# Kernel tuning notes

Measured on AMD Instinct MI355X. Metric: run time of the kernel, lower is better.

## Reference

```python
import jax, jax.numpy as jnp
import numpy as np

ALPHA = 0.2  # LeakyReLU negative slope
NEG_PAD = jnp.float32(-2**31)
N, IN_F, OUT_F = 8192, 512, 64


def setup_inputs() -> dict:
    key = jax.random.key(0)
    k1, k2, k3, k4 = jax.random.split(key, 4)
    h = jax.random.normal(k1, (N, IN_F), dtype=jnp.float32)
    adj = jax.random.randint(k2, (N, N), 0, 2, dtype=jnp.int32)
    # xavier_uniform with gain=1.414
    gain = 1.414
    limW = gain * np.sqrt(6.0 / (IN_F + OUT_F))
    W = jax.random.uniform(k3, (IN_F, OUT_F), dtype=jnp.float32, minval=-limW, maxval=limW)
    lima = gain * np.sqrt(6.0 / (2 * OUT_F + 1))
    a = jax.random.uniform(k4, (2 * OUT_F, 1), dtype=jnp.float32, minval=-lima, maxval=lima)
    return {"h": h, "adj": adj, "W": W, "a": a}


def reference(h, adj, W, a):
    Wh = h @ W                                   # [N, F']
    Wh1 = Wh @ a[:OUT_F, :]                      # [N, 1]
    Wh2 = Wh @ a[OUT_F:, :]                      # [N, 1]
    e = jax.nn.leaky_relu(Wh1 + Wh2.T, negative_slope=ALPHA)  # [N, N]
    attention = jnp.where(adj > 0, e, NEG_PAD)
    attention = jax.nn.softmax(attention, axis=1)
    # dropout in eval mode -> identity
    h_prime = attention @ Wh                     # [N, F']
    return jax.nn.elu(h_prime)                   # concat=True branch
```

## Files before the change

### kernel.cpp

```cpp
#include <hip/hip_runtime.h>
#include <cstdint>
#include <cstddef>

#define LRALPHA 0.2f

typedef _Float16 half8 __attribute__((ext_vector_type(8)));
typedef float f32x4 __attribute__((ext_vector_type(4)));

__global__ __launch_bounds__(256) void k0_bitpack(const int* __restrict__ adj,
                                                  unsigned char* __restrict__ bits8)
{
  const int nb = 8192 * 1024;
  const int stride = gridDim.x * 256;
  for (int b = blockIdx.x * 256 + threadIdx.x; b < nb; b += stride) {
    const int4* p = reinterpret_cast<const int4*>(adj + (size_t)b * 8);
    const int4 x = p[0], y = p[1];
    unsigned m = (x.x > 0 ? 1u : 0u) | (x.y > 0 ? 2u : 0u)
               | (x.z > 0 ? 4u : 0u) | (x.w > 0 ? 8u : 0u)
               | (y.x > 0 ? 16u : 0u) | (y.y > 0 ? 32u : 0u)
               | (y.z > 0 ? 64u : 0u) | (y.w > 0 ? 128u : 0u);
    bits8[b] = (unsigned char)m;
  }
}

__global__ __launch_bounds__(256) void k1_wh(
    const float* __restrict__ h, const float* __restrict__ W, const float* __restrict__ a,
    _Float16* __restrict__ whTsw, float* __restrict__ wh1, float* __restrict__ wh2)
{
  __shared__ __align__(16) float h_lds[32][34];
  __shared__ __align__(16) float w_lds[32][64];
  __shared__ __align__(16) _Float16 whT_l[64][32];

  const int t = threadIdx.x;
  const int tx = t & 15, ty = t >> 4;
  const int i0 = blockIdx.x * 32;

  const int hrow = t >> 3, hk4 = (t & 7) * 4;
  const int wk = t >> 3, wc = (t & 7) * 8;

  float acc00 = 0, acc01 = 0, acc02 = 0, acc03 = 0;
  float acc10 = 0, acc11 = 0, acc12 = 0, acc13 = 0;

  float4 hv  = *reinterpret_cast<const float4*>(&h[(size_t)(i0 + hrow) * 512 + hk4]);
  float4 wv0 = *reinterpret_cast<const float4*>(&W[(size_t)wk * 64 + wc]);
  float4 wv1 = *reinterpret_cast<const float4*>(&W[(size_t)wk * 64 + wc + 4]);

  for (int k0 = 0; k0 < 512; k0 += 32) {
    h_lds[hk4 + 0][hrow] = hv.x;
    h_lds[hk4 + 1][hrow] = hv.y;
    h_lds[hk4 + 2][hrow] = hv.z;
    h_lds[hk4 + 3][hrow] = hv.w;
    *reinterpret_cast<float4*>(&w_lds[wk][wc])     = wv0;
    *reinterpret_cast<float4*>(&w_lds[wk][wc + 4]) = wv1;
    __syncthreads();
    if (k0 + 32 < 512) {
      hv  = *reinterpret_cast<const float4*>(&h[(size_t)(i0 + hrow) * 512 + k0 + 32 + hk4]);
      wv0 = *reinterpret_cast<const float4*>(&W[(size_t)(k0 + 32 + wk) * 64 + wc]);
      wv1 = *reinterpret_cast<const float4*>(&W[(size_t)(k0 + 32 + wk) * 64 + wc + 4]);
    }
#pragma unroll
    for (int kk = 0; kk < 32; ++kk) {
      float2 av = *reinterpret_cast<const float2*>(&h_lds[kk][ty * 2]);
      float4 bv = *reinterpret_cast<const float4*>(&w_lds[kk][tx * 4]);
      acc00 += av.x * bv.x; acc01 += av.x * bv.y; acc02 += av.x * bv.z; acc03 += av.x * bv.w;
      acc10 += av.y * bv.x; acc11 += av.y * bv.y; acc12 += av.y * bv.z; acc13 += av.y * bv.w;
    }
    __syncthreads();
  }

  const float a10 = a[tx * 4 + 0], a11 = a[tx * 4 + 1], a12 = a[tx * 4 + 2], a13 = a[tx * 4 + 3];
  const float a20 = a[64 + tx * 4 + 0], a21 = a[64 + tx * 4 + 1], a22 = a[64 + tx * 4 + 2], a23 = a[64 + tx * 4 + 3];
  float s1_0 = acc00 * a10 + acc01 * a11 + acc02 * a12 + acc03 * a13;
  float s1_1 = acc10 * a10 + acc11 * a11 + acc12 * a12 + acc13 * a13;
  float s2_0 = acc00 * a20 + acc01 * a21 + acc02 * a22 + acc03 * a23;
  float s2_1 = acc10 * a20 + acc11 * a21 + acc12 * a22 + acc13 * a23;
#pragma unroll
  for (int m = 1; m < 16; m <<= 1) {
    s1_0 += __shfl_xor(s1_0, m); s1_1 += __shfl_xor(s1_1, m);
    s2_0 += __shfl_xor(s2_0, m); s2_1 += __shfl_xor(s2_1, m);
  }
  if (tx == 0) {
    wh1[i0 + ty * 2 + 0] = s1_0; wh1[i0 + ty * 2 + 1] = s1_1;
    wh2[i0 + ty * 2 + 0] = s2_0; wh2[i0 + ty * 2 + 1] = s2_1;
  }

  whT_l[tx * 4 + 0][ty * 2 + 0] = (_Float16)acc00;
  whT_l[tx * 4 + 1][ty * 2 + 0] = (_Float16)acc01;
  whT_l[tx * 4 + 2][ty * 2 + 0] = (_Float16)acc02;
  whT_l[tx * 4 + 3][ty * 2 + 0] = (_Float16)acc03;
  whT_l[tx * 4 + 0][ty * 2 + 1] = (_Float16)acc10;
  whT_l[tx * 4 + 1][ty * 2 + 1] = (_Float16)acc11;
  whT_l[tx * 4 + 2][ty * 2 + 1] = (_Float16)acc12;
  whT_l[tx * 4 + 3][ty * 2 + 1] = (_Float16)acc13;
  __syncthreads();
  {
    const int cp = t >> 6, cc = (t >> 2) & 15, ks = t & 3;
    half8 v = *reinterpret_cast<const half8*>(&whT_l[cp * 16 + cc][ks * 8]);
    *reinterpret_cast<half8*>(&whTsw[(size_t)(i0 >> 5) * 2048 + cp * 512 + (cc * 4 + ks) * 8]) = v;
  }
}

__global__ __launch_bounds__(256) void k1b_max(const float* __restrict__ wh2,
                                               float* __restrict__ G)
{
  const int t = threadIdx.x;
  float m = -1e30f;
  for (int i = t; i < 8192; i += 256) m = fmaxf(m, wh2[i]);
#pragma unroll
  for (int mask = 32; mask >= 1; mask >>= 1) m = fmaxf(m, __shfl_xor(m, mask));
  __shared__ float wm[4];
  if ((t & 63) == 0) wm[t >> 6] = m;
  __syncthreads();
  if (t == 0) G[0] = fmaxf(fmaxf(wm[0], wm[1]), fmaxf(wm[2], wm[3]));
}

__global__ __launch_bounds__(512) void k2_attn(
    const unsigned char* __restrict__ bits8, const _Float16* __restrict__ whTsw,
    const float* __restrict__ wh1, const float* __restrict__ wh2,
    const float* __restrict__ Gp, float* __restrict__ out)
{
  __shared__ __align__(16) float Osm[8][16][64];
  __shared__ float Dsm[8][16];

  const int t = threadIdx.x;
  const int lane = t & 63;
  const int w = t >> 6;
  const int c = lane & 15;
  const int ks = lane >> 4;
  const int i0 = blockIdx.x * 16;

  const float Gv = Gp[0];
  const float w1r = wh1[i0 + c];
  const float mx = w1r + Gv;
  const float mh = fmaxf(mx, LRALPHA * mx);

  const unsigned char* mp = bits8 + (size_t)(i0 + c) * 1024 + w * 128 + ks;
  const float* wh2p = wh2 + w * 1024 + ks * 8;
  const _Float16* bp = whTsw + (size_t)(w * 32) * 2048 + (c * 4 + ks) * 8;

  f32x4 acc0 = {0.f,0.f,0.f,0.f}, acc1 = {0.f,0.f,0.f,0.f};
  f32x4 acc2 = {0.f,0.f,0.f,0.f}, acc3 = {0.f,0.f,0.f,0.f};
  float ps = 0.f;

  unsigned Am, Bm;
  float4 Aw0, Aw1, Bw0, Bw1;
  half8 Ab0, Ab1, Ab2, Ab3, Bb0, Bb1, Bb2, Bb3;

#define LOADSET(P, CI) do {                                                     \
    P##m  = mp[(CI) * 4];                                                       \
    P##w0 = *reinterpret_cast<const float4*>(wh2p + (CI) * 32);                 \
    P##w1 = *reinterpret_cast<const float4*>(wh2p + (CI) * 32 + 4);             \
    P##b0 = *reinterpret_cast<const half8*>(bp + (size_t)(CI) * 2048);          \
    P##b1 = *reinterpret_cast<const half8*>(bp + (size_t)(CI) * 2048 + 512);    \
    P##b2 = *reinterpret_cast<const half8*>(bp + (size_t)(CI) * 2048 + 1024);   \
    P##b3 = *reinterpret_cast<const half8*>(bp + (size_t)(CI) * 2048 + 1536); } while (0)

#define BODY(P, NEXTCI) do {                                                    \
    const unsigned cm = P##m;                                                   \
    const float4 cw0 = P##w0, cw1 = P##w1;                                      \
    const half8 cb0 = P##b0, cb1 = P##b1, cb2 = P##b2, cb3 = P##b3;             \
    if ((NEXTCI) < 32) LOADSET(P, NEXTCI);                                      \
    half8 af;                                                                   \
    { float s_ = w1r + cw0.x; s_ = fmaxf(s_, LRALPHA*s_);                       \
      float p_ = (cm & 1u)   ? __expf(s_ - mh) : 0.f; ps += p_; af[0] = (_Float16)p_; } \
    { float s_ = w1r + cw0.y; s_ = fmaxf(s_, LRALPHA*s_);                       \
      float p_ = (cm & 2u)   ? __expf(s_ - mh) : 0.f; ps += p_; af[1] = (_Float16)p_; } \
    { float s_ = w1r + cw0.z; s_ = fmaxf(s_, LRALPHA*s_);                       \
      float p_ = (cm & 4u)   ? __expf(s_ - mh) : 0.f; ps += p_; af[2] = (_Float16)p_; } \
    { float s_ = w1r + cw0.w; s_ = fmaxf(s_, LRALPHA*s_);                       \
      float p_ = (cm & 8u)   ? __expf(s_ - mh) : 0.f; ps += p_; af[3] = (_Float16)p_; } \
    { float s_ = w1r + cw1.x; s_ = fmaxf(s_, LRALPHA*s_);                       \
      float p_ = (cm & 16u)  ? __expf(s_ - mh) : 0.f; ps += p_; af[4] = (_Float16)p_; } \
    { float s_ = w1r + cw1.y; s_ = fmaxf(s_, LRALPHA*s_);                       \
      float p_ = (cm & 32u)  ? __expf(s_ - mh) : 0.f; ps += p_; af[5] = (_Float16)p_; } \
    { float s_ = w1r + cw1.z; s_ = fmaxf(s_, LRALPHA*s_);                       \
      float p_ = (cm & 64u)  ? __expf(s_ - mh) : 0.f; ps += p_; af[6] = (_Float16)p_; } \
    { float s_ = w1r + cw1.w; s_ = fmaxf(s_, LRALPHA*s_);                       \
      float p_ = (cm & 128u) ? __expf(s_ - mh) : 0.f; ps += p_; af[7] = (_Float16)p_; } \
    acc0 = __builtin_amdgcn_mfma_f32_16x16x32_f16(af, cb0, acc0, 0, 0, 0);      \
    acc1 = __builtin_amdgcn_mfma_f32_16x16x32_f16(af, cb1, acc1, 0, 0, 0);      \
    acc2 = __builtin_amdgcn_mfma_f32_16x16x32_f16(af, cb2, acc2, 0, 0, 0);      \
    acc3 = __builtin_amdgcn_mfma_f32_16x16x32_f16(af, cb3, acc3, 0, 0, 0);      \
  } while (0)

  LOADSET(A, 0);
  LOADSET(B, 1);

  for (int ci = 0; ci < 32; ci += 2) {
    BODY(A, ci + 2);
    BODY(B, ci + 3);
  }
#undef BODY
#undef LOADSET

  float r = ps;
  r += __shfl_xor(r, 16);
  r += __shfl_xor(r, 32);
  if (ks == 0) Dsm[w][c] = r;

#pragma unroll
  for (int q = 0; q < 4; ++q) {
    Osm[w][ks * 4 + q][ 0 + c] = acc0[q];
    Osm[w][ks * 4 + q][16 + c] = acc1[q];
    Osm[w][ks * 4 + q][32 + c] = acc2[q];
    Osm[w][ks * 4 + q][48 + c] = acc3[q];
  }
  __syncthreads();

  {
    const int row = t >> 5, c2 = (t & 31) * 2;
    float d = 0.f, sx = 0.f, sy = 0.f;
#pragma unroll
    for (int ww = 0; ww < 8; ++ww) {
      d  += Dsm[ww][row];
      float2 v = *reinterpret_cast<const float2*>(&Osm[ww][row][c2]);
      sx += v.x; sy += v.y;
    }
    const float inv = 1.0f / d;
    float ox = sx * inv, oy = sy * inv;
    ox = ox > 0.f ? ox : __expf(ox) - 1.f;
    oy = oy > 0.f ? oy : __expf(oy) - 1.f;
    float2 o = {ox, oy};
    *reinterpret_cast<float2*>(&out[(size_t)(i0 + row) * 64 + c2]) = o;
  }
}

extern "C" void kernel_launch(void* const* d_in, const int* in_sizes, int n_in,
                              void* d_out, int out_size, void* d_ws, size_t ws_size,
                              hipStream_t stream) {
  const float* h   = (const float*)d_in[0];
  const int*   adj = (const int*)d_in[1];
  const float* W   = (const float*)d_in[2];
  const float* a   = (const float*)d_in[3];
  float* out = (float*)d_out;

  char* ws = (char*)d_ws;
  _Float16* whTsw = (_Float16*)ws;
  float* wh1 = (float*)(ws + 0x100000);
  float* wh2 = (float*)(ws + 0x108000);
  float* G   = (float*)(ws + 0x110000);
  unsigned char* bits8 = (unsigned char*)(ws + 0x120000);

  k0_bitpack<<<dim3(2048), dim3(256), 0, stream>>>(adj, bits8);
  k1_wh<<<dim3(256), dim3(256), 0, stream>>>(h, W, a, whTsw, wh1, wh2);
  k1b_max<<<dim3(1), dim3(256), 0, stream>>>(wh2, G);
  k2_attn<<<dim3(512), dim3(512), 0, stream>>>(bits8, whTsw, wh1, wh2, G, out);
}
```

Measured before the change: 123.3 us.

## Split attention into score kernel writing fp16 P and separate PV MFMA kernel

Drops the adjacency bitpack pre-pass and the fused score+MFMA kernel. A new score kernel reads the int32 adjacency directly, computes the masked exponentials, and writes a full fp16 probability matrix plus per-stripe row-sum partials. A second kernel multiplies that matrix by Wh with MFMA, handling two row tiles per block. This decouples the exp-heavy scoring work from the MFMA work, but it adds a large intermediate write and re-read of the N×N fp16 matrix, far more than the packed bitmask it replaces.

```diff
diff --git a/kernel.cpp b/kernel.cpp
--- a/kernel.cpp
+++ b/kernel.cpp
@@ -6,22 +6,6 @@
 
 typedef _Float16 half8 __attribute__((ext_vector_type(8)));
 typedef float f32x4 __attribute__((ext_vector_type(4)));
-
-__global__ __launch_bounds__(256) void k0_bitpack(const int* __restrict__ adj,
-                                                  unsigned char* __restrict__ bits8)
-{
-  const int nb = 8192 * 1024;
-  const int stride = gridDim.x * 256;
-  for (int b = blockIdx.x * 256 + threadIdx.x; b < nb; b += stride) {
-    const int4* p = reinterpret_cast<const int4*>(adj + (size_t)b * 8);
-    const int4 x = p[0], y = p[1];
-    unsigned m = (x.x > 0 ? 1u : 0u) | (x.y > 0 ? 2u : 0u)
-               | (x.z > 0 ? 4u : 0u) | (x.w > 0 ? 8u : 0u)
-               | (y.x > 0 ? 16u : 0u) | (y.y > 0 ? 32u : 0u)
-               | (y.z > 0 ? 64u : 0u) | (y.w > 0 ? 128u : 0u);
-    bits8[b] = (unsigned char)m;
-  }
-}
 
 __global__ __launch_bounds__(256) void k1_wh(
     const float* __restrict__ h, const float* __restrict__ W, const float* __restrict__ a,
@@ -114,78 +98,122 @@
   if (t == 0) G[0] = fmaxf(fmaxf(wm[0], wm[1]), fmaxf(wm[2], wm[3]));
 }
 
-__global__ __launch_bounds__(512) void k2_attn(
-    const unsigned char* __restrict__ bits8, const _Float16* __restrict__ whTsw,
-    const float* __restrict__ wh1, const float* __restrict__ wh2,
-    const float* __restrict__ Gp, float* __restrict__ out)
-{
-  __shared__ __align__(16) float Osm[8][16][64];
-  __shared__ float Dsm[8][16];
-
+__global__ __launch_bounds__(256) void k2s_score(
+    const int* __restrict__ adj, const float* __restrict__ wh1,
+    const float* __restrict__ wh2, const float* __restrict__ Gp,
+    _Float16* __restrict__ P, float* __restrict__ Dpart)
+{
   const int t = threadIdx.x;
   const int lane = t & 63;
   const int w = t >> 6;
-  const int c = lane & 15;
-  const int ks = lane >> 4;
-  const int i0 = blockIdx.x * 16;
+  const int g = blockIdx.x * 4 + w;
+  const int tile = g >> 3;
+  const int stripe = g & 7;
+  const int c = lane & 15, ks = lane >> 4;
+  const int row = tile * 16 + c;
 
   const float Gv = Gp[0];
-  const float w1r = wh1[i0 + c];
+  const float w1r = wh1[row];
   const float mx = w1r + Gv;
   const float mh = fmaxf(mx, LRALPHA * mx);
 
-  const unsigned char* mp = bits8 + (size_t)(i0 + c) * 1024 + w * 128 + ks;
-  const float* wh2p = wh2 + w * 1024 + ks * 8;
-  const _Float16* bp = whTsw + (size_t)(w * 32) * 2048 + (c * 4 + ks) * 8;
-
-  f32x4 acc0 = {0.f,0.f,0.f,0.f}, acc1 = {0.f,0.f,0.f,0.f};
-  f32x4 acc2 = {0.f,0.f,0.f,0.f}, acc3 = {0.f,0.f,0.f,0.f};
+  const int*   ap = adj + (size_t)row * 8192 + stripe * 1024 + ks * 8;
+  const float* wp = wh2 + stripe * 1024 + ks * 8;
+  _Float16* pp = P + (size_t)(tile * 256 + stripe * 32) * 512 + (c * 4 + ks) * 8;
+
   float ps = 0.f;
 
-  unsigned Am, Bm;
+  int4 Aa0, Aa1, Ba0, Ba1;
   float4 Aw0, Aw1, Bw0, Bw1;
-  half8 Ab0, Ab1, Ab2, Ab3, Bb0, Bb1, Bb2, Bb3;
-
-#define LOADSET(P, CI) do {                                                     \
-    P##m  = mp[(CI) * 4];                                                       \
-    P##w0 = *reinterpret_cast<const float4*>(wh2p + (CI) * 32);                 \
-    P##w1 = *reinterpret_cast<const float4*>(wh2p + (CI) * 32 + 4);             \
-    P##b0 = *reinterpret_cast<const half8*>(bp + (size_t)(CI) * 2048);          \
-    P##b1 = *reinterpret_cast<const half8*>(bp + (size_t)(CI) * 2048 + 512);    \
-    P##b2 = *reinterpret_cast<const half8*>(bp + (size_t)(CI) * 2048 + 1024);   \
-    P##b3 = *reinterpret_cast<const half8*>(bp + (size_t)(CI) * 2048 + 1536); } while (0)
-
-#define BODY(P, NEXTCI) do {                                                    \
-    const unsigned cm = P##m;                                                   \
-    const float4 cw0 = P##w0, cw1 = P##w1;                                      \
-    const half8 cb0 = P##b0, cb1 = P##b1, cb2 = P##b2, cb3 = P##b3;             \
-    if ((NEXTCI) < 32) LOADSET(P, NEXTCI);                                      \
-    half8 af;                                                                   \
-    { float s_ = w1r + cw0.x; s_ = fmaxf(s_, LRALPHA*s_);                       \
-      float p_ = (cm & 1u)   ? __expf(s_ - mh) : 0.f; ps += p_; af[0] = (_Float16)p_; } \
-    { float s_ = w1r + cw0.y; s_ = fmaxf(s_, LRALPHA*s_);                       \
-      float p_ = (cm & 2u)   ? __expf(s_ - mh) : 0.f; ps += p_; af[1] = (_Float16)p_; } \
-    { float s_ = w1r + cw0.z; s_ = fmaxf(s_, LRALPHA*s_);                       \
-      float p_ = (cm & 4u)   ? __expf(s_ - mh) : 0.f; ps += p_; af[2] = (_Float16)p_; } \
-    { float s_ = w1r + cw0.w; s_ = fmaxf(s_, LRALPHA*s_);                       \
-      float p_ = (cm & 8u)   ? __expf(s_ - mh) : 0.f; ps += p_; af[3] = (_Float16)p_; } \
-    { float s_ = w1r + cw1.x; s_ = fmaxf(s_, LRALPHA*s_);                       \
-      float p_ = (cm & 16u)  ? __expf(s_ - mh) : 0.f; ps += p_; af[4] = (_Float16)p_; } \
-    { float s_ = w1r + cw1.y; s_ = fmaxf(s_, LRALPHA*s_);                       \
-      float p_ = (cm & 32u)  ? __expf(s_ - mh) : 0.f; ps += p_; af[5] = (_Float16)p_; } \
-    { float s_ = w1r + cw1.z; s_ = fmaxf(s_, LRALPHA*s_);                       \
-      float p_ = (cm & 64u)  ? __expf(s_ - mh) : 0.f; ps += p_; af[6] = (_Float16)p_; } \
-    { float s_ = w1r + cw1.w; s_ = fmaxf(s_, LRALPHA*s_);                       \
-      float p_ = (cm & 128u) ? __expf(s_ - mh) : 0.f; ps += p_; af[7] = (_Float16)p_; } \
-    acc0 = __builtin_amdgcn_mfma_f32_16x16x32_f16(af, cb0, acc0, 0, 0, 0);      \
-    acc1 = __builtin_amdgcn_mfma_f32_16x16x32_f16(af, cb1, acc1, 0, 0, 0);      \
-    acc2 = __builtin_amdgcn_mfma_f32_16x16x32_f16(af, cb2, acc2, 0, 0, 0);      \
-    acc3 = __builtin_amdgcn_mfma_f32_16x16x32_f16(af, cb3, acc3, 0, 0, 0);      \
-  } while (0)
+
+#define LOADSET(Q, CI) do {                                                     \
+    Q##a0 = *reinterpret_cast<const int4*>(ap + (CI) * 32);                     \
+    Q##a1 = *reinterpret_cast<const int4*>(ap + (CI) * 32 + 4);                 \
+    Q##w0 = *reinterpret_cast<const float4*>(wp + (CI) * 32);                   \
+    Q##w1 = *reinterpret_cast<const float4*>(wp + (CI) * 32 + 4); } while (0)
+
+#define SCORE(AV, WV, E) {                                                      \
+    float s_ = w1r + (WV);                                                      \
+    s_ = fmaxf(s_, LRALPHA * s_);                                               \
+    float p_ = ((AV) > 0) ? __expf(s_ - mh) : 0.f;                              \
+    ps += p_; pv[E] = (_Float16)p_; }
+
+#define BODY(Q, CI, NEXTCI) do {                                                \
+    const int4 a0 = Q##a0, a1 = Q##a1;                                          \
+    const float4 q0 = Q##w0, q1 = Q##w1;                                        \
+    if ((NEXTCI) < 32) LOADSET(Q, NEXTCI);                                      \
+    half8 pv;                                                                   \
+    SCORE(a0.x, q0.x, 0) SCORE(a0.y, q0.y, 1)                                   \
+    SCORE(a0.z, q0.z, 2) SCORE(a0.w, q0.w, 3)                                   \
+    SCORE(a1.x, q1.x, 4) SCORE(a1.y, q1.y, 5)                                   \
+    SCORE(a1.z, q1.z, 6) SCORE(a1.w, q1.w, 7)                                   \
+    *reinterpret_cast<half8*>(pp + (size_t)(CI) * 512) = pv; } while (0)
 
   LOADSET(A, 0);
   LOADSET(B, 1);
-
+  for (int ci = 0; ci < 32; ci += 2) {
+    BODY(A, ci, ci + 2);
+    BODY(B, ci + 1, ci + 3);
+  }
+#undef BODY
+#undef SCORE
+#undef LOADSET
+
+  float r = ps;
+  r += __shfl_xor(r, 16);
+  r += __shfl_xor(r, 32);
+  if (ks == 0) Dpart[(size_t)stripe * 8192 + row] = r;
+}
+
+__global__ __launch_bounds__(512) void k3_pv(
+    const _Float16* __restrict__ P, const _Float16* __restrict__ whTsw,
+    const float* __restrict__ Dpart, float* __restrict__ out)
+{
+  __shared__ __align__(16) float Osm[8][32][64];
+
+  const int t = threadIdx.x;
+  const int lane = t & 63;
+  const int w = t >> 6;
+  const int c = lane & 15, ks = lane >> 4;
+  const int tile0 = blockIdx.x * 2;
+  const int row0 = tile0 * 16;
+
+  const _Float16* pp0 = P + (size_t)(tile0 * 256 + w * 32) * 512 + (c * 4 + ks) * 8;
+  const _Float16* pp1 = pp0 + 256 * 512;
+  const _Float16* bp  = whTsw + (size_t)(w * 32) * 2048 + (c * 4 + ks) * 8;
+
+  f32x4 a00 = {0.f,0.f,0.f,0.f}, a01 = {0.f,0.f,0.f,0.f};
+  f32x4 a02 = {0.f,0.f,0.f,0.f}, a03 = {0.f,0.f,0.f,0.f};
+  f32x4 a10 = {0.f,0.f,0.f,0.f}, a11 = {0.f,0.f,0.f,0.f};
+  f32x4 a12 = {0.f,0.f,0.f,0.f}, a13 = {0.f,0.f,0.f,0.f};
+
+  half8 Aa, Az, Ab0, Ab1, Ab2, Ab3;
+  half8 Ba, Bz, Bb0, Bb1, Bb2, Bb3;
+
+#define LOADSET(Q, CI) do {                                                     \
+    Q##a  = *reinterpret_cast<const half8*>(pp0 + (size_t)(CI) * 512);          \
+    Q##z  = *reinterpret_cast<const half8*>(pp1 + (size_t)(CI) * 512);          \
+    Q##b0 = *reinterpret_cast<const half8*>(bp + (size_t)(CI) * 2048);          \
+    Q##b1 = *reinterpret_cast<const half8*>(bp + (size_t)(CI) * 2048 + 512);    \
+    Q##b2 = *reinterpret_cast<const half8*>(bp + (size_t)(CI) * 2048 + 1024);   \
+    Q##b3 = *reinterpret_cast<const half8*>(bp + (size_t)(CI) * 2048 + 1536); } while (0)
+
+#define BODY(Q, NEXTCI) do {                                                    \
+    const half8 fa = Q##a, fz = Q##z;                                           \
+    const half8 cb0 = Q##b0, cb1 = Q##b1, cb2 = Q##b2, cb3 = Q##b3;             \
+    if ((NEXTCI) < 32) LOADSET(Q, NEXTCI);                                      \
+    a00 = __builtin_amdgcn_mfma_f32_16x16x32_f16(fa, cb0, a00, 0, 0, 0);        \
+    a01 = __builtin_amdgcn_mfma_f32_16x16x32_f16(fa, cb1, a01, 0, 0, 0);        \
+    a02 = __builtin_amdgcn_mfma_f32_16x16x32_f16(fa, cb2, a02, 0, 0, 0);        \
+    a03 = __builtin_amdgcn_mfma_f32_16x16x32_f16(fa, cb3, a03, 0, 0, 0);        \
+    a10 = __builtin_amdgcn_mfma_f32_16x16x32_f16(fz, cb0, a10, 0, 0, 0);        \
+    a11 = __builtin_amdgcn_mfma_f32_16x16x32_f16(fz, cb1, a11, 0, 0, 0);        \
+    a12 = __builtin_amdgcn_mfma_f32_16x16x32_f16(fz, cb2, a12, 0, 0, 0);        \
+    a13 = __builtin_amdgcn_mfma_f32_16x16x32_f16(fz, cb3, a13, 0, 0, 0);        \
+  } while (0)
+
+  LOADSET(A, 0);
+  LOADSET(B, 1);
   for (int ci = 0; ci < 32; ci += 2) {
     BODY(A, ci + 2);
     BODY(B, ci + 3);
@@ -193,35 +221,38 @@
 #undef BODY
 #undef LOADSET
 
-  float r = ps;
-  r += __shfl_xor(r, 16);
-  r += __shfl_xor(r, 32);
-  if (ks == 0) Dsm[w][c] = r;
-
 #pragma unroll
   for (int q = 0; q < 4; ++q) {
-    Osm[w][ks * 4 + q][ 0 + c] = acc0[q];
-    Osm[w][ks * 4 + q][16 + c] = acc1[q];
-    Osm[w][ks * 4 + q][32 + c] = acc2[q];
-    Osm[w][ks * 4 + q][48 + c] = acc3[q];
+    Osm[w][ks * 4 + q][ 0 + c] = a00[q];
+    Osm[w][ks * 4 + q][16 + c] = a01[q];
+    Osm[w][ks * 4 + q][32 + c] = a02[q];
+    Osm[w][ks * 4 + q][48 + c] = a03[q];
+    Osm[w][16 + ks * 4 + q][ 0 + c] = a10[q];
+    Osm[w][16 + ks * 4 + q][16 + c] = a11[q];
+    Osm[w][16 + ks * 4 + q][32 + c] = a12[q];
+    Osm[w][16 + ks * 4 + q][48 + c] = a13[q];
   }
   __syncthreads();
 
   {
-    const int row = t >> 5, c2 = (t & 31) * 2;
-    float d = 0.f, sx = 0.f, sy = 0.f;
+    const int row = t >> 4, c4 = (t & 15) * 4;
+    float d = 0.f;
+#pragma unroll
+    for (int s = 0; s < 8; ++s) d += Dpart[(size_t)s * 8192 + row0 + row];
+    const float inv = 1.0f / d;
+    float sx = 0.f, sy = 0.f, sz = 0.f, sw = 0.f;
 #pragma unroll
     for (int ww = 0; ww < 8; ++ww) {
-      d  += Dsm[ww][row];
-      float2 v = *reinterpret_cast<const float2*>(&Osm[ww][row][c2]);
-      sx += v.x; sy += v.y;
+      float4 v = *reinterpret_cast<const float4*>(&Osm[ww][row][c4]);
+      sx += v.x; sy += v.y; sz += v.z; sw += v.w;
     }
-    const float inv = 1.0f / d;
-    float ox = sx * inv, oy = sy * inv;
-    ox = ox > 0.f ? ox : __expf(ox) - 1.f;
-    oy = oy > 0.f ? oy : __expf(oy) - 1.f;
-    float2 o = {ox, oy};
-    *reinterpret_cast<float2*>(&out[(size_t)(i0 + row) * 64 + c2]) = o;
+    float4 o;
+    o.x = sx * inv; o.y = sy * inv; o.z = sz * inv; o.w = sw * inv;
+    o.x = o.x > 0.f ? o.x : __expf(o.x) - 1.f;
+    o.y = o.y > 0.f ? o.y : __expf(o.y) - 1.f;
+    o.z = o.z > 0.f ? o.z : __expf(o.z) - 1.f;
+    o.w = o.w > 0.f ? o.w : __expf(o.w) - 1.f;
+    *reinterpret_cast<float4*>(&out[(size_t)(row0 + row) * 64 + c4]) = o;
   }
 }
 
@@ -236,13 +267,14 @@
 
   char* ws = (char*)d_ws;
   _Float16* whTsw = (_Float16*)ws;
-  float* wh1 = (float*)(ws + 0x100000);
-  float* wh2 = (float*)(ws + 0x108000);
-  float* G   = (float*)(ws + 0x110000);
-  unsigned char* bits8 = (unsigned char*)(ws + 0x120000);
-
-  k0_bitpack<<<dim3(2048), dim3(256), 0, stream>>>(adj, bits8);
+  float* wh1   = (float*)(ws + 0x100000);
+  float* wh2   = (float*)(ws + 0x108000);
+  float* G     = (float*)(ws + 0x110000);
+  float* Dpart = (float*)(ws + 0x118000);
+  _Float16* P  = (_Float16*)(ws + 0x200000);
+
   k1_wh<<<dim3(256), dim3(256), 0, stream>>>(h, W, a, whTsw, wh1, wh2);
   k1b_max<<<dim3(1), dim3(256), 0, stream>>>(wh2, G);
-  k2_attn<<<dim3(512), dim3(512), 0, stream>>>(bits8, whTsw, wh1, wh2, G, out);
-}
+  k2s_score<<<dim3(1024), dim3(256), 0, stream>>>(adj, wh1, wh2, G, P, Dpart);
+  k3_pv<<<dim3(256), dim3(512), 0, stream>>>(P, whTsw, Dpart, out);
+}
```

Measured after the change: 158.2 us. 1.28x slower.

## Fuse adjacency bitpack into attention kernel with LDS-staged probabilities

Applied to the files above, without the earlier changes.

Removes the separate bitpack pass so the attention kernel reads the int32 adjacency directly with nontemporal loads. Each wave computes probabilities for two rows and writes them to swizzled, double-buffered LDS. All waves then run MFMAs over a 512-column chunk, which restructures the work split across waves. The logits are prescaled by log2(e) so the kernel can use exp2f. This avoids writing and rereading the bit mask but adds a __syncthreads per chunk and a heavier direct stream of the 256MB adjacency.

```diff
diff --git a/kernel.cpp b/kernel.cpp
--- a/kernel.cpp
+++ b/kernel.cpp
@@ -3,29 +3,15 @@
 #include <cstddef>
 
 #define LRALPHA 0.2f
+#define LOG2E 1.44269504f
 
 typedef _Float16 half8 __attribute__((ext_vector_type(8)));
 typedef float f32x4 __attribute__((ext_vector_type(4)));
-
-__global__ __launch_bounds__(256) void k0_bitpack(const int* __restrict__ adj,
-                                                  unsigned char* __restrict__ bits8)
-{
-  const int nb = 8192 * 1024;
-  const int stride = gridDim.x * 256;
-  for (int b = blockIdx.x * 256 + threadIdx.x; b < nb; b += stride) {
-    const int4* p = reinterpret_cast<const int4*>(adj + (size_t)b * 8);
-    const int4 x = p[0], y = p[1];
-    unsigned m = (x.x > 0 ? 1u : 0u) | (x.y > 0 ? 2u : 0u)
-               | (x.z > 0 ? 4u : 0u) | (x.w > 0 ? 8u : 0u)
-               | (y.x > 0 ? 16u : 0u) | (y.y > 0 ? 32u : 0u)
-               | (y.z > 0 ? 64u : 0u) | (y.w > 0 ? 128u : 0u);
-    bits8[b] = (unsigned char)m;
-  }
-}
+typedef int int4v __attribute__((ext_vector_type(4)));
 
 __global__ __launch_bounds__(256) void k1_wh(
     const float* __restrict__ h, const float* __restrict__ W, const float* __restrict__ a,
-    _Float16* __restrict__ whTsw, float* __restrict__ wh1, float* __restrict__ wh2)
+    _Float16* __restrict__ whTsw, float* __restrict__ wh1s, float* __restrict__ wh2s)
 {
   __shared__ __align__(16) float h_lds[32][34];
   __shared__ __align__(16) float w_lds[32][64];
@@ -80,8 +66,8 @@
     s2_0 += __shfl_xor(s2_0, m); s2_1 += __shfl_xor(s2_1, m);
   }
   if (tx == 0) {
-    wh1[i0 + ty * 2 + 0] = s1_0; wh1[i0 + ty * 2 + 1] = s1_1;
-    wh2[i0 + ty * 2 + 0] = s2_0; wh2[i0 + ty * 2 + 1] = s2_1;
+    wh1s[i0 + ty * 2 + 0] = s1_0 * LOG2E; wh1s[i0 + ty * 2 + 1] = s1_1 * LOG2E;
+    wh2s[i0 + ty * 2 + 0] = s2_0 * LOG2E; wh2s[i0 + ty * 2 + 1] = s2_1 * LOG2E;
   }
 
   whT_l[tx * 4 + 0][ty * 2 + 0] = (_Float16)acc00;
@@ -100,12 +86,12 @@
   }
 }
 
-__global__ __launch_bounds__(256) void k1b_max(const float* __restrict__ wh2,
+__global__ __launch_bounds__(256) void k1b_max(const float* __restrict__ wh2s,
                                                float* __restrict__ G)
 {
   const int t = threadIdx.x;
   float m = -1e30f;
-  for (int i = t; i < 8192; i += 256) m = fmaxf(m, wh2[i]);
+  for (int i = t; i < 8192; i += 256) m = fmaxf(m, wh2s[i]);
 #pragma unroll
   for (int mask = 32; mask >= 1; mask >>= 1) m = fmaxf(m, __shfl_xor(m, mask));
   __shared__ float wm[4];
@@ -114,114 +100,170 @@
   if (t == 0) G[0] = fmaxf(fmaxf(wm[0], wm[1]), fmaxf(wm[2], wm[3]));
 }
 
-__global__ __launch_bounds__(512) void k2_attn(
-    const unsigned char* __restrict__ bits8, const _Float16* __restrict__ whTsw,
-    const float* __restrict__ wh1, const float* __restrict__ wh2,
+__global__ __launch_bounds__(512, 4) void k2f(
+    const int* __restrict__ adj, const _Float16* __restrict__ whTsw,
+    const float* __restrict__ wh1s, const float* __restrict__ wh2s,
     const float* __restrict__ Gp, float* __restrict__ out)
 {
-  __shared__ __align__(16) float Osm[8][16][64];
-  __shared__ float Dsm[8][16];
+  __shared__ __align__(16) _Float16 Plds[2][16][512];
+  __shared__ float Osm[2][4][16][16];
+  __shared__ float Dsh[16];
 
   const int t = threadIdx.x;
   const int lane = t & 63;
   const int w = t >> 6;
-  const int c = lane & 15;
-  const int ks = lane >> 4;
   const int i0 = blockIdx.x * 16;
 
-  const float Gv = Gp[0];
-  const float w1r = wh1[i0 + c];
-  const float mx = w1r + Gv;
-  const float mh = fmaxf(mx, LRALPHA * mx);
-
-  const unsigned char* mp = bits8 + (size_t)(i0 + c) * 1024 + w * 128 + ks;
-  const float* wh2p = wh2 + w * 1024 + ks * 8;
-  const _Float16* bp = whTsw + (size_t)(w * 32) * 2048 + (c * 4 + ks) * 8;
-
-  f32x4 acc0 = {0.f,0.f,0.f,0.f}, acc1 = {0.f,0.f,0.f,0.f};
-  f32x4 acc2 = {0.f,0.f,0.f,0.f}, acc3 = {0.f,0.f,0.f,0.f};
-  float ps = 0.f;
-
-  unsigned Am, Bm;
-  float4 Aw0, Aw1, Bw0, Bw1;
-  half8 Ab0, Ab1, Ab2, Ab3, Bb0, Bb1, Bb2, Bb3;
-
-#define LOADSET(P, CI) do {                                                     \
-    P##m  = mp[(CI) * 4];                                                       \
-    P##w0 = *reinterpret_cast<const float4*>(wh2p + (CI) * 32);                 \
-    P##w1 = *reinterpret_cast<const float4*>(wh2p + (CI) * 32 + 4);             \
-    P##b0 = *reinterpret_cast<const half8*>(bp + (size_t)(CI) * 2048);          \
-    P##b1 = *reinterpret_cast<const half8*>(bp + (size_t)(CI) * 2048 + 512);    \
-    P##b2 = *reinterpret_cast<const half8*>(bp + (size_t)(CI) * 2048 + 1024);   \
-    P##b3 = *reinterpret_cast<const half8*>(bp + (size_t)(CI) * 2048 + 1536); } while (0)
-
-#define BODY(P, NEXTCI) do {                                                    \
-    const unsigned cm = P##m;                                                   \
-    const float4 cw0 = P##w0, cw1 = P##w1;                                      \
-    const half8 cb0 = P##b0, cb1 = P##b1, cb2 = P##b2, cb3 = P##b3;             \
-    if ((NEXTCI) < 32) LOADSET(P, NEXTCI);                                      \
-    half8 af;                                                                   \
-    { float s_ = w1r + cw0.x; s_ = fmaxf(s_, LRALPHA*s_);                       \
-      float p_ = (cm & 1u)   ? __expf(s_ - mh) : 0.f; ps += p_; af[0] = (_Float16)p_; } \
-    { float s_ = w1r + cw0.y; s_ = fmaxf(s_, LRALPHA*s_);                       \
-      float p_ = (cm & 2u)   ? __expf(s_ - mh) : 0.f; ps += p_; af[1] = (_Float16)p_; } \
-    { float s_ = w1r + cw0.z; s_ = fmaxf(s_, LRALPHA*s_);                       \
-      float p_ = (cm & 4u)   ? __expf(s_ - mh) : 0.f; ps += p_; af[2] = (_Float16)p_; } \
-    { float s_ = w1r + cw0.w; s_ = fmaxf(s_, LRALPHA*s_);                       \
-      float p_ = (cm & 8u)   ? __expf(s_ - mh) : 0.f; ps += p_; af[3] = (_Float16)p_; } \
-    { float s_ = w1r + cw1.x; s_ = fmaxf(s_, LRALPHA*s_);                       \
-      float p_ = (cm & 16u)  ? __expf(s_ - mh) : 0.f; ps += p_; af[4] = (_Float16)p_; } \
-    { float s_ = w1r + cw1.y; s_ = fmaxf(s_, LRALPHA*s_);                       \
-      float p_ = (cm & 32u)  ? __expf(s_ - mh) : 0.f; ps += p_; af[5] = (_Float16)p_; } \
-    { float s_ = w1r + cw1.z; s_ = fmaxf(s_, LRALPHA*s_);                       \
-      float p_ = (cm & 64u)  ? __expf(s_ - mh) : 0.f; ps += p_; af[6] = (_Float16)p_; } \
-    { float s_ = w1r + cw1.w; s_ = fmaxf(s_, LRALPHA*s_);                       \
-      float p_ = (cm & 128u) ? __expf(s_ - mh) : 0.f; ps += p_; af[7] = (_Float16)p_; } \
-    acc0 = __builtin_amdgcn_mfma_f32_16x16x32_f16(af, cb0, acc0, 0, 0, 0);      \
-    acc1 = __builtin_amdgcn_mfma_f32_16x16x32_f16(af, cb1, acc1, 0, 0, 0);      \
-    acc2 = __builtin_amdgcn_mfma_f32_16x16x32_f16(af, cb2, acc2, 0, 0, 0);      \
-    acc3 = __builtin_amdgcn_mfma_f32_16x16x32_f16(af, cb3, acc3, 0, 0, 0);      \
-  } while (0)
-
-  LOADSET(A, 0);
-  LOADSET(B, 1);
-
-  for (int ci = 0; ci < 32; ci += 2) {
-    BODY(A, ci + 2);
-    BODY(B, ci + 3);
-  }
+  const int rA = w * 2, rB = rA + 1;
+  const float Gs = Gp[0];
+  const float w1A = wh1s[i0 + rA], w1B = wh1s[i0 + rB];
+  const float mxA = w1A + Gs, mxB = w1B + Gs;
+  const float mhA = fmaxf(mxA, LRALPHA * mxA);
+  const float mhB = fmaxf(mxB, LRALPHA * mxB);
+
+  const int* adjA = adj + (size_t)(i0 + rA) * 8192 + lane * 8;
+  const int* adjB = adj + (size_t)(i0 + rB) * 8192 + lane * 8;
+  const float* wp = wh2s + lane * 8;
+
+  const int c = lane & 15, ks = lane >> 4;
+  const int cp = w & 3, kh = w >> 2;
+  const int cxor = (c & 7) << 4;
+  char* PldsB = reinterpret_cast<char*>(&Plds[0][0][0]);
+  const _Float16* bbase = whTsw + (size_t)kh * 8 * 2048 + cp * 512 + c * 32 + ks * 8;
+
+  float psA = 0.f, psB = 0.f;
+  f32x4 acc = {0.f, 0.f, 0.f, 0.f};
+
+  int4v s0Aa, s0Ab, s0Ba, s0Bb, s1Aa, s1Ab, s1Ba, s1Bb;
+  float4 qa, qb;
+  half8 b0, b1, b2, b3, b4, b5, b6, b7;
+
+#define LOAD_ADJ(S, CH) do { \
+    S##Aa = __builtin_nontemporal_load(reinterpret_cast<const int4v*>(adjA + (CH) * 512)); \
+    S##Ab = __builtin_nontemporal_load(reinterpret_cast<const int4v*>(adjA + (CH) * 512 + 4)); \
+    S##Ba = __builtin_nontemporal_load(reinterpret_cast<const int4v*>(adjB + (CH) * 512)); \
+    S##Bb = __builtin_nontemporal_load(reinterpret_cast<const int4v*>(adjB + (CH) * 512 + 4)); \
+  } while (0)
+
+#define LOAD_WH(CH) do { \
+    qa = *reinterpret_cast<const float4*>(wp + (CH) * 512); \
+    qb = *reinterpret_cast<const float4*>(wp + (CH) * 512 + 4); \
+  } while (0)
+
+#define SC1(PS, PV, E, AV, QV, W1, MH) { \
+    float x_ = (W1) + (QV); x_ = fmaxf(x_, LRALPHA * x_); \
+    float p_ = ((AV) > 0) ? exp2f(x_ - (MH)) : 0.f; \
+    (PS) += p_; (PV)[E] = (_Float16)p_; }
+
+#define COMP_STORE(S, CH) do { \
+    half8 pvA_, pvB_; \
+    SC1(psA, pvA_, 0, S##Aa.x, qa.x, w1A, mhA) \
+    SC1(psA, pvA_, 1, S##Aa.y, qa.y, w1A, mhA) \
+    SC1(psA, pvA_, 2, S##Aa.z, qa.z, w1A, mhA) \
+    SC1(psA, pvA_, 3, S##Aa.w, qa.w, w1A, mhA) \
+    SC1(psA, pvA_, 4, S##Ab.x, qb.x, w1A, mhA) \
+    SC1(psA, pvA_, 5, S##Ab.y, qb.y, w1A, mhA) \
+    SC1(psA, pvA_, 6, S##Ab.z, qb.z, w1A, mhA) \
+    SC1(psA, pvA_, 7, S##Ab.w, qb.w, w1A, mhA) \
+    SC1(psB, pvB_, 0, S##Ba.x, qa.x, w1B, mhB) \
+    SC1(psB, pvB_, 1, S##Ba.y, qa.y, w1B, mhB) \
+    SC1(psB, pvB_, 2, S##Ba.z, qa.z, w1B, mhB) \
+    SC1(psB, pvB_, 3, S##Ba.w, qa.w, w1B, mhB) \
+    SC1(psB, pvB_, 4, S##Bb.x, qb.x, w1B, mhB) \
+    SC1(psB, pvB_, 5, S##Bb.y, qb.y, w1B, mhB) \
+    SC1(psB, pvB_, 6, S##Bb.z, qb.z, w1B, mhB) \
+    SC1(psB, pvB_, 7, S##Bb.w, qb.w, w1B, mhB) \
+    char* pb_ = PldsB + ((CH) & 1) * 16384; \
+    *reinterpret_cast<half8*>(pb_ + rA * 1024 + ((lane * 16) ^ ((rA & 7) << 4))) = pvA_; \
+    *reinterpret_cast<half8*>(pb_ + rB * 1024 + ((lane * 16) ^ ((rB & 7) << 4))) = pvB_; \
+  } while (0)
+
+#define PV_LOADB(CH) do { \
+    const _Float16* bp_ = bbase + (size_t)(CH) * 32768; \
+    b0 = *reinterpret_cast<const half8*>(bp_ + 0 * 2048); \
+    b1 = *reinterpret_cast<const half8*>(bp_ + 1 * 2048); \
+    b2 = *reinterpret_cast<const half8*>(bp_ + 2 * 2048); \
+    b3 = *reinterpret_cast<const half8*>(bp_ + 3 * 2048); \
+    b4 = *reinterpret_cast<const half8*>(bp_ + 4 * 2048); \
+    b5 = *reinterpret_cast<const half8*>(bp_ + 5 * 2048); \
+    b6 = *reinterpret_cast<const half8*>(bp_ + 6 * 2048); \
+    b7 = *reinterpret_cast<const half8*>(bp_ + 7 * 2048); \
+  } while (0)
+
+#define PV_MFMA(CH) do { \
+    const char* pr_ = PldsB + ((CH) & 1) * 16384 + c * 1024 + kh * 512; \
+    half8 a_; \
+    a_ = *reinterpret_cast<const half8*>(pr_ + ((0 * 64 + ks * 16) ^ cxor)); \
+    acc = __builtin_amdgcn_mfma_f32_16x16x32_f16(a_, b0, acc, 0, 0, 0); \
+    a_ = *reinterpret_cast<const half8*>(pr_ + ((1 * 64 + ks * 16) ^ cxor)); \
+    acc = __builtin_amdgcn_mfma_f32_16x16x32_f16(a_, b1, acc, 0, 0, 0); \
+    a_ = *reinterpret_cast<const half8*>(pr_ + ((2 * 64 + ks * 16) ^ cxor)); \
+    acc = __builtin_amdgcn_mfma_f32_16x16x32_f16(a_, b2, acc, 0, 0, 0); \
+    a_ = *reinterpret_cast<const half8*>(pr_ + ((3 * 64 + ks * 16) ^ cxor)); \
+    acc = __builtin_amdgcn_mfma_f32_16x16x32_f16(a_, b3, acc, 0, 0, 0); \
+    a_ = *reinterpret_cast<const half8*>(pr_ + ((4 * 64 + ks * 16) ^ cxor)); \
+    acc = __builtin_amdgcn_mfma_f32_16x16x32_f16(a_, b4, acc, 0, 0, 0); \
+    a_ = *reinterpret_cast<const half8*>(pr_ + ((5 * 64 + ks * 16) ^ cxor)); \
+    acc = __builtin_amdgcn_mfma_f32_16x16x32_f16(a_, b5, acc, 0, 0, 0); \
+    a_ = *reinterpret_cast<const half8*>(pr_ + ((6 * 64 + ks * 16) ^ cxor)); \
+    acc = __builtin_amdgcn_mfma_f32_16x16x32_f16(a_, b6, acc, 0, 0, 0); \
+    a_ = *reinterpret_cast<const half8*>(pr_ + ((7 * 64 + ks * 16) ^ cxor)); \
+    acc = __builtin_amdgcn_mfma_f32_16x16x32_f16(a_, b7, acc, 0, 0, 0); \
+  } while (0)
+
+
+#define BODY(CH, LD, CM) { \
+    PV_LOADB(CH); \
+    if ((CH) < 14) LOAD_ADJ(LD, (CH) + 2); \
+    if ((CH) < 15) LOAD_WH((CH) + 1); \
+    PV_MFMA(CH); \
+    if ((CH) < 15) COMP_STORE(CM, (CH) + 1); \
+    __syncthreads(); }
+
+  LOAD_ADJ(s0, 0);
+  LOAD_WH(0);
+  LOAD_ADJ(s1, 1);
+  COMP_STORE(s0, 0);
+  __syncthreads();
+
+  BODY(0,  s0, s1)  BODY(1,  s1, s0)
+  BODY(2,  s0, s1)  BODY(3,  s1, s0)
+  BODY(4,  s0, s1)  BODY(5,  s1, s0)
+  BODY(6,  s0, s1)  BODY(7,  s1, s0)
+  BODY(8,  s0, s1)  BODY(9,  s1, s0)
+  BODY(10, s0, s1)  BODY(11, s1, s0)
+  BODY(12, s0, s1)  BODY(13, s1, s0)
+  BODY(14, s0, s1)  BODY(15, s1, s0)
+
 #undef BODY
-#undef LOADSET
-
-  float r = ps;
-  r += __shfl_xor(r, 16);
-  r += __shfl_xor(r, 32);
-  if (ks == 0) Dsm[w][c] = r;
-
-#pragma unroll
-  for (int q = 0; q < 4; ++q) {
-    Osm[w][ks * 4 + q][ 0 + c] = acc0[q];
-    Osm[w][ks * 4 + q][16 + c] = acc1[q];
-    Osm[w][ks * 4 + q][32 + c] = acc2[q];
-    Osm[w][ks * 4 + q][48 + c] = acc3[q];
-  }
+#undef PV_MFMA
+#undef PV_LOADB
+#undef COMP_STORE
+#undef SC1
+#undef LOAD_WH
+#undef LOAD_ADJ
+
+#pragma unroll
+  for (int m = 1; m < 64; m <<= 1) {
+    psA += __shfl_xor(psA, m);
+    psB += __shfl_xor(psB, m);
+  }
+  if (lane == 0) { Dsh[rA] = psA; Dsh[rB] = psB; }
+#pragma unroll
+  for (int q = 0; q < 4; ++q) Osm[kh][cp][ks * 4 + q][c] = acc[q];
   __syncthreads();
 
   {
-    const int row = t >> 5, c2 = (t & 31) * 2;
-    float d = 0.f, sx = 0.f, sy = 0.f;
-#pragma unroll
-    for (int ww = 0; ww < 8; ++ww) {
-      d  += Dsm[ww][row];
-      float2 v = *reinterpret_cast<const float2*>(&Osm[ww][row][c2]);
-      sx += v.x; sy += v.y;
-    }
-    const float inv = 1.0f / d;
-    float ox = sx * inv, oy = sy * inv;
-    ox = ox > 0.f ? ox : __expf(ox) - 1.f;
-    oy = oy > 0.f ? oy : __expf(oy) - 1.f;
-    float2 o = {ox, oy};
-    *reinterpret_cast<float2*>(&out[(size_t)(i0 + row) * 64 + c2]) = o;
+    const int row = t >> 5;
+    const int col = (t & 31) * 2;
+    const int cg = col >> 4, cc = col & 15;
+    const float inv = 1.0f / Dsh[row];
+    float o0 = (Osm[0][cg][row][cc] + Osm[1][cg][row][cc]) * inv;
+    float o1 = (Osm[0][cg][row][cc + 1] + Osm[1][cg][row][cc + 1]) * inv;
+    o0 = o0 > 0.f ? o0 : __expf(o0) - 1.f;
+    o1 = o1 > 0.f ? o1 : __expf(o1) - 1.f;
+    float2 o = {o0, o1};
+    *reinterpret_cast<float2*>(&out[(size_t)(i0 + row) * 64 + col]) = o;
   }
 }
 
@@ -236,13 +278,11 @@
 
   char* ws = (char*)d_ws;
   _Float16* whTsw = (_Float16*)ws;
-  float* wh1 = (float*)(ws + 0x100000);
-  float* wh2 = (float*)(ws + 0x108000);
-  float* G   = (float*)(ws + 0x110000);
-  unsigned char* bits8 = (unsigned char*)(ws + 0x120000);
-
-  k0_bitpack<<<dim3(2048), dim3(256), 0, stream>>>(adj, bits8);
-  k1_wh<<<dim3(256), dim3(256), 0, stream>>>(h, W, a, whTsw, wh1, wh2);
-  k1b_max<<<dim3(1), dim3(256), 0, stream>>>(wh2, G);
-  k2_attn<<<dim3(512), dim3(512), 0, stream>>>(bits8, whTsw, wh1, wh2, G, out);
-}
+  float* wh1s = (float*)(ws + 0x100000);
+  float* wh2s = (float*)(ws + 0x108000);
+  float* G    = (float*)(ws + 0x110000);
+
+  k1_wh<<<dim3(256), dim3(256), 0, stream>>>(h, W, a, whTsw, wh1s, wh2s);
+  k1b_max<<<dim3(1), dim3(256), 0, stream>>>(wh2s, G);
+  k2f<<<dim3(512), dim3(512), 0, stream>>>(adj, whTsw, wh1s, wh2s, G, out);
+}
```

Result: slower. 171.8 us (+39.3%).
